# Performance work log

Measured on AMD Instinct MI355X. Metric: run time of the kernel, lower is better.

The kernel has to match this reference:

```python
import jax, jax.numpy as jnp
import numpy as np

# ---- static config (mirrors GaussianLSS __init__) ----
ORF_H, ORF_W = 256, 704
FC, FH, FW = 128, 32, 88
D_ST, D_END, D_STEP = 4.0, 45.0, 1.0
OUT_C = 128
ERROR_TOL = 1.0
OPACITY_THR = 0.05
XB = (-50.0, 50.0, 1.0)
YB = (-50.0, 50.0, 1.0)
BEV_H = int(round((YB[1] - YB[0]) / YB[2]))
BEV_W = int(round((XB[1] - XB[0]) / XB[2]))
DS = np.arange(D_ST, D_END, D_STEP, dtype=np.float32)
D = DS.shape[0]  # 41
BN_EPS = 1e-3
CHUNK = 512      # gaussians composited per scan step (16896 = 33*512)
B, NCAM = 1, 6


def make_frustum():
    ds = jnp.broadcast_to(jnp.asarray(DS)[:, None, None], (D, FH, FW))
    xs = jnp.broadcast_to(jnp.linspace(0.0, ORF_W - 1.0, FW)[None, None, :], (D, FH, FW))
    ys = jnp.broadcast_to(jnp.linspace(0.0, ORF_H - 1.0, FH)[None, :, None], (D, FH, FW))
    return jnp.stack([xs, ys, ds], -1)  # [D,FH,FW,3]


def get_geometry(rots, trans, intrins, post_rots, post_trans):
    fr = make_frustum()
    pts = fr[None, None] - post_trans[:, :, None, None, None, :]
    pts = jnp.einsum('bnij,bndhwj->bndhwi', jnp.linalg.inv(post_rots), pts)
    pts = jnp.concatenate([pts[..., :2] * pts[..., 2:3], pts[..., 2:3]], -1)
    comb = jnp.einsum('bnij,bnjk->bnik', rots, jnp.linalg.inv(intrins))
    pts = jnp.einsum('bnij,bndhwj->bndhwi', comb, pts) + trans[:, :, None, None, None, :]
    return pts  # [B,N,D,FH,FW,3] ego-frame frustum points


def conv2d(x, w, b, pad):
    y = jax.lax.conv_general_dilated(x, w, (1, 1), [(pad, pad), (pad, pad)],
                                     dimension_numbers=('NCHW', 'OIHW', 'NCHW'))
    return y + b[None, :, None, None]


def bnorm(x, g, bt, m, v):
    s = (g / jnp.sqrt(v + BN_EPS))[None, :, None, None]
    return (x - m[None, :, None, None]) * s + bt[None, :, None, None]


def splat(means, cov6, colors, ops, valid_in):
    # Differentiable BEV gaussian rasterization (3DGS math, orthographic BEV camera,
    # all depths equal -> compositing in stable gaussian-index order).
    H, W = BEV_H, BEV_W
    sh, sw = H / 2.0, W / 2.0  # h/h_meters with FoV=2 (BEVCamera)
    my = -sh * means[:, 1] + H / 2.0  # pixel row (full_proj_transform row 0)
    mx = -sw * means[:, 0] + W / 2.0  # pixel col (row 1)
    a = sh * sh * cov6[:, 3] + 0.3    # 2D cov = J Sigma_xy J^T, +0.3 low-pass as in 3DGS
    c = sw * sw * cov6[:, 0] + 0.3
    b = sh * sw * cov6[:, 1]
    det = a * c - b * b
    valid = valid_in & (det > 0)
    inv_det = jnp.where(det > 0, 1.0 / det, 0.0)
    cA, cB, cC = c * inv_det, -b * inv_det, a * inv_det
    pi = jnp.repeat(jnp.arange(H, dtype=jnp.float32), W)  # [P] pixel rows
    pj = jnp.tile(jnp.arange(W, dtype=jnp.float32), H)    # [P] pixel cols
    G = means.shape[0]
    nchunk = G // CHUNK
    resh = lambda x: x.reshape((nchunk, CHUNK) + x.shape[1:])
    chunks = (resh(my), resh(mx), resh(cA), resh(cB), resh(cC),
              resh(ops), resh(valid), resh(colors))

    def body(carry, ch):
        logT, acc = carry
        my_c, mx_c, A, Bc, Cc, op_c, val_c, col_c = ch
        dI = pi[None, :] - my_c[:, None]                     # [Gc,P]
        dJ = pj[None, :] - mx_c[:, None]
        q = A[:, None] * dI * dI + 2.0 * Bc[:, None] * dI * dJ + Cc[:, None] * dJ * dJ
        alpha = jnp.minimum(0.99, op_c[:, None] * jnp.exp(-0.5 * q))
        alpha = jnp.where(val_c[:, None] & (q >= 0) & (alpha >= 1.0 / 255.0), alpha, 0.0)
        log1m = jnp.log1p(-alpha)
        cum = jnp.cumsum(log1m, axis=0)
        T = jnp.exp(logT[None, :] + cum - log1m)             # transmittance before each gaussian
        acc = acc + jnp.einsum('gp,gc->pc', alpha * T, col_c)
        return (logT + cum[-1], acc), None

    P = H * W
    init = (jnp.zeros((P,), jnp.float32), jnp.zeros((P, colors.shape[1]), jnp.float32))
    (_, acc), _ = jax.lax.scan(jax.checkpoint(body), init, chunks)
    return acc.reshape(H, W, -1).transpose(2, 0, 1)  # [C,H,W], bg is zeros


def _forward(cam2ego_rot, cam2ego_trans, cam_intrins, post_cam2ego_rot, post_cam2ego_trans,
             img_feats, conv1_w, conv1_b, bn1_g, bn1_b, bn1_m, bn1_v,
             conv2_w, conv2_b, bn2_g, bn2_b, bn2_m, bn2_v, conv3_w, conv3_b):
    geom = get_geometry(cam2ego_rot, cam2ego_trans, cam_intrins, post_cam2ego_rot, post_cam2ego_trans)
    b, n = img_feats.shape[:2]
    x = img_feats.reshape(b * n, FC, FH, FW)
    x = jax.nn.relu(bnorm(conv2d(x, conv1_w, conv1_b, 1), bn1_g, bn1_b, bn1_m, bn1_v))
    x = jax.nn.relu(bnorm(conv2d(x, conv2_w, conv2_b, 1), bn2_g, bn2_b, bn2_m, bn2_v))
    x = conv2d(x, conv3_w, conv3_b, 0)
    depth_prob = jax.nn.softmax(x[:, :D], axis=1).reshape(b, n, D, FH, FW)
    opac = jax.nn.sigmoid(x[:, D:D + 1]).reshape(b, n, FH, FW)
    feats = x[:, D + 1:].reshape(b, n, OUT_C, FH, FW)
    # per-pixel gaussian moments of the depth distribution (compute_gaussian)
    means = jnp.einsum('bndhw,bndhwi->bnhwi', depth_prob, geom)
    delta = means[:, :, None] - geom                                       # [B,N,D,FH,FW,3]
    cov = jnp.einsum('bndhw,bndhwi,bndhwj->bnhwij', depth_prob, delta, delta) * (ERROR_TOL ** 2 / 9.0)
    center = jnp.array([(XB[0] + XB[1]) / 2.0, (YB[0] + YB[1]) / 2.0, 0.0], jnp.float32)
    scale = jnp.array([2.0 / (XB[1] - XB[0]), 2.0 / (YB[1] - YB[0]), 1.0], jnp.float32)
    m_n = (means - center) * scale
    cov_n = cov * (scale[:, None] * scale[None, :])
    cov6 = jnp.stack([cov_n[..., 0, 0], cov_n[..., 0, 1], cov_n[..., 0, 2],
                      cov_n[..., 1, 1], cov_n[..., 1, 2], cov_n[..., 2, 2]], -1)
    g = n * FH * FW
    colors = feats.transpose(0, 1, 3, 4, 2).reshape(b, g, OUT_C)
    m_n = m_n.reshape(b, g, 3)
    cov6 = cov6.reshape(b, g, 6)
    ops = opac.reshape(b, g)
    mask = ops > OPACITY_THR  # opacity filtering == zero contribution, order preserved
    bev = jax.vmap(splat)(m_n, cov6, colors, ops, mask)                    # [B,C,H,W]
    num_gaussians = mask.astype(jnp.float32).sum(-1).mean()
    return bev, num_gaussians


def setup_inputs():
    key = jax.random.key(0)
    ks = jax.random.split(key, 8)
    # camera-to-ego rotations: cam->ego axis permutation composed with per-camera yaw
    yaw = np.linspace(0.0, 2.0 * np.pi, NCAM, endpoint=False).astype(np.float32)
    cz, sz = np.cos(yaw), np.sin(yaw)
    rotz = np.zeros((NCAM, 3, 3), np.float32)
    rotz[:, 0, 0] = cz; rotz[:, 0, 1] = -sz
    rotz[:, 1, 0] = sz; rotz[:, 1, 1] = cz
    rotz[:, 2, 2] = 1.0
    perm = np.array([[0.0, 0.0, 1.0], [-1.0, 0.0, 0.0], [0.0, -1.0, 0.0]], np.float32)
    rots = np.einsum('nij,jk->nik', rotz, perm)
    cam2ego_rot = jnp.asarray(np.broadcast_to(rots, (B, NCAM, 3, 3)).copy())
    cam2ego_trans = jax.random.normal(ks[0], (B, NCAM, 3), jnp.float32)
    K = np.array([[600.0, 0.0, ORF_W / 2.0], [0.0, 600.0, ORF_H / 2.0], [0.0, 0.0, 1.0]], np.float32)
    cam_intrins = jnp.asarray(np.broadcast_to(K, (B, NCAM, 3, 3)).copy())
    post_cam2ego_rot = jnp.broadcast_to(jnp.eye(3, dtype=jnp.float32), (B, NCAM, 3, 3)) + jnp.zeros((B, NCAM, 3, 3), jnp.float32)
    post_cam2ego_trans = jnp.zeros((B, NCAM, 3), jnp.float32)
    img_feats = jax.random.normal(ks[1], (B, NCAM, FC, FH, FW), jnp.float32)
    def conv_init(k, o, i, kh, kw):
        return jax.random.normal(k, (o, i, kh, kw), jnp.float32) * (1.0 / np.sqrt(i * kh * kw))
    return dict(cam2ego_rot=cam2ego_rot, cam2ego_trans=cam2ego_trans, cam_intrins=cam_intrins,
                post_cam2ego_rot=post_cam2ego_rot, post_cam2ego_trans=post_cam2ego_trans,
                img_feats=img_feats,
                conv1_w=conv_init(ks[2], FC, FC, 3, 3), conv1_b=jnp.zeros((FC,), jnp.float32),
                bn1_g=jnp.ones((FC,), jnp.float32), bn1_b=jnp.zeros((FC,), jnp.float32),
                bn1_m=jnp.zeros((FC,), jnp.float32), bn1_v=jnp.ones((FC,), jnp.float32),
                conv2_w=conv_init(ks[3], FC, FC, 3, 3), conv2_b=jnp.zeros((FC,), jnp.float32),
                bn2_g=jnp.ones((FC,), jnp.float32), bn2_b=jnp.zeros((FC,), jnp.float32),
                bn2_m=jnp.zeros((FC,), jnp.float32), bn2_v=jnp.ones((FC,), jnp.float32),
                conv3_w=conv_init(ks[4], OUT_C + D + 1, FC, 1, 1),
                conv3_b=jax.random.normal(ks[5], (OUT_C + D + 1,), jnp.float32) * 0.1)


def reference(cam2ego_rot, cam2ego_trans, cam_intrins, post_cam2ego_rot, post_cam2ego_trans,
              img_feats, conv1_w, conv1_b, bn1_g, bn1_b, bn1_m, bn1_v,
              conv2_w, conv2_b, bn2_g, bn2_b, bn2_m, bn2_v, conv3_w, conv3_b):
    return _forward(cam2ego_rot, cam2ego_trans, cam_intrins, post_cam2ego_rot, post_cam2ego_trans,
                    img_feats, conv1_w, conv1_b, bn1_g, bn1_b, bn1_m, bn1_v,
                    conv2_w, conv2_b, bn2_g, bn2_b, bn2_m, bn2_v, conv3_w, conv3_b)
```

## Files before the change

kernel.cpp:

```cpp
#include <hip/hip_runtime.h>

#define NCAM 6
#define FC   128
#define FH_  32
#define FW_  88
#define NPIX (FH_*FW_)
#define PH   34
#define PW   92
#define PPIX (PH*PW)
#define ND   41
#define X3D  42
#define OUTC 128
#define GTOT (NCAM*NPIX)
#define BEVH 100
#define BEVW 100
#define NPXB (BEVH*BEVW)
#define NTILE 25
#define NWORD 264
#define NMASKW (NTILE*NTILE*NWORD)
#define WCAP  70000
#define CSIZE 64
#define CBLK  2048

#define SZA     (NCAM*FC*PPIX)
#define WS_CAM  0
#define WS_A    256
#define WS_RB   (WS_A  + SZA)
#define WS_X3   (WS_RB + SZA)
#define WS_GS   (WS_X3 + NCAM*X3D*NPIX)
#define WS_WL   (WS_GS + GTOT*8)
#define WS_BASE (WS_WL + WCAP)

__device__ inline void inv3x3(const float* m, float* o) {
    float a=m[0],b=m[1],c=m[2],d=m[3],e=m[4],f=m[5],g=m[6],h=m[7],i=m[8];
    float A=e*i-f*h, B=c*h-b*i, C=b*f-c*e;
    float Dd=f*g-d*i, E=a*i-c*g, F=c*d-a*f;
    float Gg=d*h-e*g, H=b*g-a*h, I=a*e-b*d;
    float r = 1.0f/(a*A + b*Dd + c*Gg);
    o[0]=A*r; o[1]=B*r; o[2]=C*r; o[3]=Dd*r; o[4]=E*r; o[5]=F*r;
    o[6]=Gg*r; o[7]=H*r; o[8]=I*r;
}

__global__ __launch_bounds__(256) void pad_input_kernel(const float* __restrict__ src,
        float* __restrict__ dst, float* __restrict__ rb,
        float* __restrict__ outp, unsigned long long* __restrict__ masks) {
    int idx = blockIdx.x*256 + threadIdx.x;
    if (idx < NMASKW) masks[idx] = 0ull;
    if (idx <= NPXB*OUTC) outp[idx] = 0.0f;
    if (idx >= NCAM*FC*PPIX) return;
    int plane = idx / PPIX, pp = idx - plane*PPIX;
    int y = pp / PW, x = pp - y*PW;
    bool interior = (y >= 1 && y <= FH_ && x >= 1 && x <= FW_);
    float v = 0.0f;
    if (interior)
        v = src[(size_t)plane*NPIX + (y-1)*FW_ + (x-1)];
    dst[idx] = v;
    if (!interior) rb[idx] = 0.0f;
}

__global__ __launch_bounds__(128) void conv3x3_pf_kernel(
        const float* __restrict__ in, float* __restrict__ out, const float* __restrict__ w,
        const float* __restrict__ cb, const float* __restrict__ bg, const float* __restrict__ bb,
        const float* __restrict__ bm, const float* __restrict__ bv) {
    const int n   = blockIdx.x;
    const int co0 = blockIdx.y * 4;
    const int qid = blockIdx.z * 128 + threadIdx.x;
    if (qid >= 704) return;
    const int y = qid / 22, x0 = (qid - y*22) * 4;
    float scale[4], shift[4];
    #pragma unroll
    for (int c=0;c<4;c++) {
        float s = bg[co0+c] * rsqrtf(bv[co0+c] + 1e-3f);
        scale[c] = s;
        shift[c] = (cb[co0+c] - bm[co0+c]) * s + bb[co0+c];
    }
    float acc[4][4] = {};
    const float* ip = in + (size_t)n*FC*PPIX + y*PW + x0;
    const float* wb = w + (size_t)co0*FC*9;
    float4 p4[3]; float2 p2[3];
    #pragma unroll
    for (int r=0;r<3;r++) {
        p4[r] = *(const float4*)(ip + r*PW);
        p2[r] = *(const float2*)(ip + r*PW + 4);
    }
    for (int ci=0; ci<FC; ++ci) {
        float v[3][6];
        #pragma unroll
        for (int r=0;r<3;r++) {
            v[r][0]=p4[r].x; v[r][1]=p4[r].y; v[r][2]=p4[r].z; v[r][3]=p4[r].w;
            v[r][4]=p2[r].x; v[r][5]=p2[r].y;
        }
        if (ci + 1 < FC) {
            const float* ipn = ip + PPIX;
            #pragma unroll
            for (int r=0;r<3;r++) {
                p4[r] = *(const float4*)(ipn + r*PW);
                p2[r] = *(const float2*)(ipn + r*PW + 4);
            }
        }
        #pragma unroll
        for (int c=0;c<4;c++) {
            const float* wr = wb + (size_t)c*FC*9 + ci*9;
            float w00=wr[0],w01=wr[1],w02=wr[2],w10=wr[3],w11=wr[4],
                  w12=wr[5],w20=wr[6],w21=wr[7],w22=wr[8];
            #pragma unroll
            for (int p=0;p<4;p++) {
                float a = acc[c][p];
                a = fmaf(w00, v[0][p], a); a = fmaf(w01, v[0][p+1], a); a = fmaf(w02, v[0][p+2], a);
                a = fmaf(w10, v[1][p], a); a = fmaf(w11, v[1][p+1], a); a = fmaf(w12, v[1][p+2], a);
                a = fmaf(w20, v[2][p], a); a = fmaf(w21, v[2][p+1], a); a = fmaf(w22, v[2][p+2], a);
                acc[c][p] = a;
            }
        }
        ip += PPIX;
    }
    const int po = (y+1)*PW + (x0+1);
    #pragma unroll
    for (int c=0;c<4;c++) {
        float* op = out + ((size_t)n*FC + co0 + c)*PPIX + po;
        #pragma unroll
        for (int p=0;p<4;p++)
            op[p] = fmaxf(fmaf(acc[c][p], scale[c], shift[c]), 0.0f);
    }
}

__global__ __launch_bounds__(256) void conv1x1_kernel(const float* __restrict__ in,
        float* __restrict__ x3d, float* __restrict__ colors,
        const float* __restrict__ w, const float* __restrict__ b) {
    const int n   = blockIdx.x;
    const int px  = blockIdx.y * 256 + threadIdx.x;
    const int y   = px / FW_, x = px - y*FW_;
    const int pp  = (y+1)*PW + (x+1);
    const float* ip = in + (size_t)n*FC*PPIX + pp;
    if (blockIdx.z < 6) {
        const int co0 = blockIdx.z * 7;
        const float* wr[7];
        float acc[7];
        #pragma unroll
        for (int k=0;k<7;k++) {
            int co = co0 + k;
            wr[k]  = w + (size_t)co*FC;
            acc[k] = b[co];
        }
        #pragma unroll 4
        for (int ci=0; ci<FC; ++ci) {
            float v = ip[(size_t)ci*PPIX];
            #pragma unroll
            for (int k=0;k<7;k++) acc[k] = fmaf(wr[k][ci], v, acc[k]);
        }
        #pragma unroll
        for (int k=0;k<7;k++)
            x3d[((size_t)n*X3D + co0 + k)*NPIX + px] = acc[k];
    } else {
        const int c0  = (blockIdx.z - 6) * 8;
        const int co0 = X3D + c0;
        const float* wr[8];
        float acc[8];
        #pragma unroll
        for (int k=0;k<8;k++) {
            int co = co0 + k;
            wr[k]  = w + (size_t)co*FC;
            acc[k] = b[co];
        }
        #pragma unroll 4
        for (int ci=0; ci<FC; ++ci) {
            float v = ip[(size_t)ci*PPIX];
            #pragma unroll
            for (int k=0;k<8;k++) acc[k] = fmaf(wr[k][ci], v, acc[k]);
        }
        float* cp = colors + (((size_t)(n*NPIX + px)) << 7) + c0;
        *(float4*)(cp)     = make_float4(acc[0], acc[1], acc[2], acc[3]);
        *(float4*)(cp + 4) = make_float4(acc[4], acc[5], acc[6], acc[7]);
    }
}

__global__ __launch_bounds__(256) void moments_kernel(const float* __restrict__ x3,
        const float* __restrict__ rot, const float* __restrict__ tr,
        const float* __restrict__ intr, const float* __restrict__ prot,
        const float* __restrict__ ptr_, float* __restrict__ gauss,
        float* __restrict__ ng) {
    __shared__ float cc[24];
    const int n = blockIdx.x / 11;
    if (threadIdx.x == 0) {
        float M1[9], Ki[9];
        inv3x3(prot + n*9, M1);
        inv3x3(intr + n*9, Ki);
        const float* R = rot + n*9;
        #pragma unroll
        for (int i=0;i<9;i++) cc[i] = M1[i];
        #pragma unroll
        for (int i=0;i<3;i++) cc[9+i] = ptr_[n*3+i];
        #pragma unroll
        for (int i=0;i<3;i++)
            #pragma unroll
            for (int j=0;j<3;j++)
                cc[12+i*3+j] = R[i*3+0]*Ki[0+j] + R[i*3+1]*Ki[3+j] + R[i*3+2]*Ki[6+j];
        #pragma unroll
        for (int i=0;i<3;i++) cc[21+i] = tr[n*3+i];
    }
    __syncthreads();
    const int gi = blockIdx.x*256 + threadIdx.x;
    const int p  = gi - n*NPIX;
    const int h  = p / FW_, xp = p - h*FW_;
    float u = xp * (703.0f/87.0f);
    float v = h  * (255.0f/31.0f);
    float fx = u - cc[9], fy = v - cc[10], fz = -cc[11];
    float p0x = cc[0]*fx + cc[1]*fy + cc[2]*fz;
    float p0y = cc[3]*fx + cc[4]*fy + cc[5]*fz;
    float p0z = cc[6]*fx + cc[7]*fy + cc[8]*fz;
    const float* lg = x3 + (size_t)n*X3D*NPIX + p;

    float lgv[ND];
    #pragma unroll
    for (int d=0; d<ND; ++d) lgv[d] = lg[(size_t)d*NPIX];

    float mxl = -1e30f;
    #pragma unroll
    for (int d=0; d<ND; ++d) mxl = fmaxf(mxl, lgv[d]);

    float s=0.f, sgx=0.f, sgy=0.f;
    #pragma unroll
    for (int d=0; d<ND; ++d) {
        float e  = __expf(lgv[d] - mxl);
        lgv[d] = e;
        float dz = 4.0f + (float)d;
        float pz = p0z + dz*cc[8];
        float px = (p0x + dz*cc[2]) * pz;
        float py = (p0y + dz*cc[5]) * pz;
        float gx = cc[12]*px + cc[13]*py + cc[14]*pz + cc[21];
        float gy = cc[15]*px + cc[16]*py + cc[17]*pz + cc[22];
        s += e; sgx += e*gx; sgy += e*gy;
    }
    float inv_s = 1.0f/s;
    float mex = sgx*inv_s, mey = sgy*inv_s;
    float cxx=0.f, cxy=0.f, cyy=0.f;
    #pragma unroll
    for (int d=0; d<ND; ++d) {
        float e  = lgv[d];
        float dz = 4.0f + (float)d;
        float pz = p0z + dz*cc[8];
        float px = (p0x + dz*cc[2]) * pz;
        float py = (p0y + dz*cc[5]) * pz;
        float gx = cc[12]*px + cc[13]*py + cc[14]*pz + cc[21];
        float gy = cc[15]*px + cc[16]*py + cc[17]*pz + cc[22];
        float dxv = gx - mex, dyv = gy - mey;
        cxx += e*dxv*dxv; cxy += e*dxv*dyv; cyy += e*dyv*dyv;
    }
    const float k9 = inv_s * (1.0f/9.0f);
    cxx *= k9; cxy *= k9; cyy *= k9;

    float lo = lg[(size_t)ND*NPIX];
    float op = 1.0f/(1.0f + __expf(-lo));
    bool mask = op > 0.05f;

    const float SC = 0.02f, SH = 50.0f, SW = 50.0f;
    float my = -SH*(mey*SC) + 50.0f;
    float mx = -SW*(mex*SC) + 50.0f;
    float a  = SH*SH*(cyy*SC*SC) + 0.3f;
    float b  = SH*SW*(cxy*SC*SC);
    float c  = SW*SW*(cxx*SC*SC) + 0.3f;
    float det = a*c - b*b;
    bool valid = mask && (det > 0.0f);
    float A, B2, C, qm, ri, rj;
    if (valid) {
        float idet = 1.0f/det;
        A = c*idet; B2 = -2.0f*b*idet; C = a*idet;
        qm = 2.0f*__logf(255.0f*op);
        ri = sqrtf(qm*a); rj = sqrtf(qm*c);
    } else { A=B2=C=0.f; qm=-1.0f; ri=-1e30f; rj=-1e30f; }
    float* gp = gauss + (size_t)gi*8;
    gp[0]=my; gp[1]=mx; gp[2]=A; gp[3]=B2; gp[4]=C; gp[5]=qm; gp[6]=ri; gp[7]=rj;

    unsigned long long bal = __ballot(mask);
    if ((threadIdx.x & 63) == 0) atomicAdd(ng, (float)__popcll(bal));
}

__global__ __launch_bounds__(256) void scatter_masks_kernel(const float* __restrict__ gauss,
        unsigned long long* __restrict__ masks) {
    const int idx = blockIdx.x*256 + threadIdx.x;
    const int g = idx >> 2, q = idx & 3;
    const float4 g0 = *(const float4*)(gauss + ((size_t)g << 3));
    const float4 g1 = *(const float4*)(gauss + ((size_t)g << 3) + 4);
    if (g1.y < 0.0f) return;
    const float my = g0.x, mx = g0.y, A = g0.z, B = 0.5f*g0.w, C = g1.x, qm = g1.y, ri = g1.z;
    const float invC = 1.0f / C;
    const float k2 = C*A - B*B;
    int ti0 = max(0, (int)floorf((my - ri) * 0.25f));
    int ti1 = min(NTILE-1, (int)floorf((my + ri) * 0.25f));
    int len = ti1 - ti0 + 1;
    int ta = ti0 + (len*q) / 4;
    int tb = ti0 + (len*(q+1)) / 4;
    const int wi = g >> 6;
    const unsigned long long bit = 1ull << (g & 63);
    for (int ti = ta; ti < tb; ++ti) {
        float jmn = 1e30f, jmx = -1e30f;
        #pragma unroll
        for (int r = 0; r < 4; ++r) {
            int i = 4*ti + r;
            if (i < 0 || i > 99) continue;
            float di = (float)i - my;
            float disc = C*qm - k2*di*di;
            if (disc < 0.0f) continue;
            float sd = sqrtf(disc);
            float jc = -B*di;
            jmn = fminf(jmn, (jc - sd)*invC + mx);
            jmx = fmaxf(jmx, (jc + sd)*invC + mx);
        }
        if (jmx < jmn) continue;
        int jl = max(0, (int)ceilf(jmn));
        int jh = min(99, (int)floorf(jmx));
        if (jl > jh) continue;
        for (int tj = (jl >> 2); tj <= (jh >> 2); ++tj)
            atomicOr(&masks[(size_t)(ti*NTILE + tj)*NWORD + wi], bit);
    }
}

__global__ __launch_bounds__(256) void cnt_kernel(const unsigned long long* __restrict__ masks,
                                                  int* __restrict__ cnt) {
    __shared__ int sc;
    const int tile = blockIdx.x, t = threadIdx.x;
    if (t == 0) sc = 0;
    __syncthreads();
    if (t < NWORD) atomicAdd(&sc, __popcll(masks[(size_t)tile*NWORD + t]));
    __syncthreads();
    if (t == 0) cnt[tile] = sc;
}

__global__ __launch_bounds__(640) void scan_kernel(const int* __restrict__ cnt,
        int* __restrict__ off, int* __restrict__ choff, int* __restrict__ nwork) {
    __shared__ int wsum[16], wsum2[16];
    const int t = threadIdx.x;
    const int lane = t & 63, wv = t >> 6;
    int c  = (t < NTILE*NTILE) ? cnt[t] : 0;
    int ch = (c + CSIZE-1) >> 6;
    int v = c, v2 = ch;
    #pragma unroll
    for (int o = 1; o < 64; o <<= 1) {
        int u  = __shfl_up(v,  (unsigned)o, 64);
        int u2 = __shfl_up(v2, (unsigned)o, 64);
        if (lane >= o) { v += u; v2 += u2; }
    }
    if (lane == 63) { wsum[wv] = v; wsum2[wv] = v2; }
    __syncthreads();
    int pre = 0, pre2 = 0;
    for (int w2 = 0; w2 < wv; ++w2) { pre += wsum[w2]; pre2 += wsum2[w2]; }
    int inc = v + pre, inc2 = v2 + pre2;
    if (t < NTILE*NTILE) { off[t] = inc - c; choff[t] = inc2 - ch; }
    if (t == NTILE*NTILE - 1) {
        off[NTILE*NTILE] = inc;
        choff[NTILE*NTILE] = inc2;
        nwork[0] = (inc2 > WCAP) ? WCAP : inc2;
    }
}

__global__ __launch_bounds__(256) void fill_kernel(const unsigned long long* __restrict__ masks,
        const int* __restrict__ cnt, const int* __restrict__ off, const int* __restrict__ choff,
        unsigned short* __restrict__ list, int* __restrict__ wl) {
    __shared__ unsigned long long sw[NWORD];
    __shared__ int wpre[NWORD];
    const int tile = blockIdx.x, t = threadIdx.x;
    if (t < NWORD) sw[t] = masks[(size_t)tile*NWORD + t];
    __syncthreads();
    if (t == 0) {
        int run = 0;
        for (int w2 = 0; w2 < NWORD; ++w2) { wpre[w2] = run; run += __popcll(sw[w2]); }
    }
    __syncthreads();
    if (t < NWORD) {
        unsigned long long m = sw[t];
        int pos = off[tile] + wpre[t], base = t << 6;
        while (m) { int b = __builtin_ctzll(m); m &= m - 1; list[pos++] = (unsigned short)(base + b); }
    }
    int nch = (cnt[tile] + CSIZE-1)/CSIZE;
    int c0 = choff[tile];
    if (t < nch && c0 + t < WCAP) wl[c0 + t] = (tile << 9) | t;
}

__device__ inline float eval_alpha(const float4 g0, const float4 g1, float fi, float fj) {
    float dI = fi - g0.x, dJ = fj - g0.y;
    float q = dI*(g0.z*dI + g0.w*dJ) + g1.x*dJ*dJ;
    if (q < 0.0f || q > g1.y) return 0.0f;
    return fminf(0.99f, 0.003921568627f * __expf(0.5f*(g1.y - q)));
}

__global__ __launch_bounds__(256) void chunk_sums_kernel(const float* __restrict__ gauss,
        const unsigned short* __restrict__ list, const int* __restrict__ cnt,
        const int* __restrict__ off, const int* __restrict__ wl, const int* __restrict__ nwork,
        float* __restrict__ base) {
    const int nw = nwork[0];
    const int lane = threadIdx.x & 63;
    const int wid  = (blockIdx.x * 256 + threadIdx.x) >> 6;
    const int nwv  = (gridDim.x * 256) >> 6;
    const int px = lane & 15, kg = lane >> 4;
    for (int e = wid; e < nw; e += nwv) {
        int v = wl[e], tile = v >> 9, c = v & 511;
        int hbase = off[tile] + (c << 6);
        int nh = min(CSIZE, cnt[tile] - (c << 6));
        const int i0 = (tile / NTILE) * 4, j0 = (tile % NTILE) * 4;
        const float fi = (float)(i0 + (px >> 2)), fj = (float)(j0 + (px & 3));
        float s = 1.0f;
        for (int k = kg; k < nh; k += 4) {
            int g = list[hbase + k];
            float4 g0 = *(const float4*)(gauss + ((size_t)g << 3));
            float4 g1 = *(const float4*)(gauss + ((size_t)g << 3) + 4);
            float a = eval_alpha(g0, g1, fi, fj);
            s *= (1.0f - a);
        }
        s *= __shfl_xor(s, 16, 64);
        s *= __shfl_xor(s, 32, 64);
        if (lane < 16) base[(size_t)e*16 + lane] = s;
    }
}

__global__ __launch_bounds__(256) void chunk_prefix_kernel(const int* __restrict__ choff,
                                                           float* __restrict__ base) {
    __shared__ float part[16][17];
    const int tile = blockIdx.x, t = threadIdx.x;
    const int c0 = choff[tile], nch = choff[tile+1] - c0;
    if (nch == 0) return;
    const int px = t & 15, cg = t >> 4;
    const int L16 = (nch + 15) >> 4;
    const int a0 = cg*L16, a1 = min(nch, a0 + L16);
    float s = 1.0f;
    for (int c = a0; c < a1; ++c) s *= base[(size_t)(c0 + c)*16 + px];
    part[cg][px] = s;
    __syncthreads();
    if (t < 16) {
        float run = 1.0f;
        #pragma unroll
        for (int k = 0; k < 16; ++k) { float tmp = part[k][t]; part[k][t] = run; run *= tmp; }
    }
    __syncthreads();
    float run = part[cg][px];
    for (int c = a0; c < a1; ++c) {
        size_t idx = (size_t)(c0 + c)*16 + px;
        float tmp = base[idx];
        base[idx] = run;
        run *= tmp;
    }
}

__global__ __launch_bounds__(256) void composite_kernel(const float* __restrict__ gauss,
        const float* __restrict__ colors, const unsigned short* __restrict__ list,
        const int* __restrict__ cnt, const int* __restrict__ off, const int* __restrict__ wl,
        const int* __restrict__ nwork, const float* __restrict__ base, float* __restrict__ out) {
    const int nw = nwork[0];
    const int t = threadIdx.x;
    const int lane = t & 63;
    const int e_px = t >> 4, e_kg = t & 15;
    const int cs4 = t & 31;
    const int par = (t >> 5) & 1;
    const int pq  = t >> 6;
    const int f_pxq = t >> 5;
    const int f_r0  = f_pxq >> 2, f_j = f_pxq & 3;
    __shared__ unsigned short slist[2][CSIZE];
    __shared__ float s_w[CSIZE][17];
    __shared__ float fred[128*17];
    const int per = (nw + CBLK - 1) / CBLK;
    int e0 = blockIdx.x * per;
    if (e0 >= nw) return;
    int e1 = min(nw, e0 + per);

    float4 acc[4];
    #pragma unroll
    for (int j=0;j<4;j++) acc[j] = make_float4(0.f,0.f,0.f,0.f);
    int cur_tile = wl[e0] >> 9;
    int cur_i0 = (cur_tile / NTILE) * 4, cur_j0 = (cur_tile % NTILE) * 4;

    int buf = 0;
    {
        int v = wl[e0], tl = v >> 9, c = v & 511;
        int nh0 = min(CSIZE, cnt[tl] - (c << 6));
        if (t < nh0) slist[0][t] = list[off[tl] + (c << 6) + t];
    }

    for (int e = e0; e < e1; ++e) {
        int v = wl[e], tile = v >> 9, c = v & 511;
        const bool tflush = (tile != cur_tile);
        const int fi0 = cur_i0, fj0 = cur_j0;
        if (tflush) {
            #pragma unroll
            for (int j = 0; j < 4; ++j) {
                acc[j].x += __shfl_xor(acc[j].x, 32, 64);
                acc[j].y += __shfl_xor(acc[j].y, 32, 64);
                acc[j].z += __shfl_xor(acc[j].z, 32, 64);
                acc[j].w += __shfl_xor(acc[j].w, 32, 64);
            }
            if (par == 0) {
                float* fr = &fred[(pq*32 + cs4)*17];
                #pragma unroll
                for (int j = 0; j < 4; ++j) {
                    fr[(j<<2)+0] = acc[j].x; fr[(j<<2)+1] = acc[j].y;
                    fr[(j<<2)+2] = acc[j].z; fr[(j<<2)+3] = acc[j].w;
                }
            }
            #pragma unroll
            for (int j=0;j<4;j++) acc[j] = make_float4(0.f,0.f,0.f,0.f);
            cur_tile = tile;
            cur_i0 = (tile / NTILE) * 4; cur_j0 = (tile % NTILE) * 4;
        }
        const int nh = min(CSIZE, cnt[tile] - (c << 6));
        __syncthreads();
        if (tflush) {
            const float* f0 = &fred[(f_r0*32 + cs4)*17 + (f_j<<2)];
            const float* f1 = &fred[((f_r0+2)*32 + cs4)*17 + (f_j<<2)];
            const int pix0 = (fi0 + f_r0) * BEVW + fj0 + f_j;
            const int pix1 = pix0 + 2 * BEVW;
            float* op = out + (size_t)(cs4 << 2) * NPXB;
            atomicAdd(op + 0*NPXB + pix0, f0[0]); atomicAdd(op + 1*NPXB + pix0, f0[1]);
            atomicAdd(op + 2*NPXB + pix0, f0[2]); atomicAdd(op + 3*NPXB + pix0, f0[3]);
            atomicAdd(op + 0*NPXB + pix1, f1[0]); atomicAdd(op + 1*NPXB + pix1, f1[1]);
            atomicAdd(op + 2*NPXB + pix1, f1[2]); atomicAdd(op + 3*NPXB + pix1, f1[3]);
        }
        if (e + 1 < e1) {
            int v2 = wl[e+1], tl2 = v2 >> 9, c2 = v2 & 511;
            int nh2 = min(CSIZE, cnt[tl2] - (c2 << 6));
            if (t < nh2) slist[buf^1][t] = list[off[tl2] + (c2 << 6) + t];
        }
        {
            const float fi = (float)(cur_i0 + (e_px >> 2)), fj = (float)(cur_j0 + (e_px & 3));
            const int k0 = e_kg << 2;
            float a4[4]; float p = 1.0f;
            #pragma unroll
            for (int i = 0; i < 4; ++i) {
                int k = k0 + i;
                float a = 0.0f;
                if (k < nh) {
                    int g = slist[buf][k];
                    float4 g0 = *(const float4*)(gauss + ((size_t)g << 3));
                    float4 g1 = *(const float4*)(gauss + ((size_t)g << 3) + 4);
                    a = eval_alpha(g0, g1, fi, fj);
                }
                a4[i] = a;
                p *= (1.0f - a);
            }
            float s = p;
            #pragma unroll
            for (int o = 1; o < 16; o <<= 1) {
                float u = __shfl_up(s, (unsigned)o, 64);
                if ((lane & 15) >= o) s *= u;
            }
            float ex = __shfl_up(s, 1u, 64);
            float T = base[(size_t)e*16 + e_px] * (((lane & 15) == 0) ? 1.0f : ex);
            #pragma unroll
            for (int i = 0; i < 4; ++i) {
                float wv = a4[i] * T; T -= wv;
                s_w[k0 + i][e_px] = wv;
            }
        }
        __syncthreads();
        if (nh == CSIZE) {
            #pragma unroll 8
            for (int k = 0; k < CSIZE/2; ++k) {
                const int idx = (k << 1) | par;
                int g = slist[buf][idx];
                const float* swr = s_w[idx] + (pq << 2);
                float w0 = swr[0], w1 = swr[1], w2 = swr[2], w3 = swr[3];
                float4 cl = *(const float4*)(colors + ((size_t)g << 7) + (cs4 << 2));
                acc[0].x = fmaf(w0, cl.x, acc[0].x); acc[0].y = fmaf(w0, cl.y, acc[0].y);
                acc[0].z = fmaf(w0, cl.z, acc[0].z); acc[0].w = fmaf(w0, cl.w, acc[0].w);
                acc[1].x = fmaf(w1, cl.x, acc[1].x); acc[1].y = fmaf(w1, cl.y, acc[1].y);
                acc[1].z = fmaf(w1, cl.z, acc[1].z); acc[1].w = fmaf(w1, cl.w, acc[1].w);
                acc[2].x = fmaf(w2, cl.x, acc[2].x); acc[2].y = fmaf(w2, cl.y, acc[2].y);
                acc[2].z = fmaf(w2, cl.z, acc[2].z); acc[2].w = fmaf(w2, cl.w, acc[2].w);
                acc[3].x = fmaf(w3, cl.x, acc[3].x); acc[3].y = fmaf(w3, cl.y, acc[3].y);
                acc[3].z = fmaf(w3, cl.z, acc[3].z); acc[3].w = fmaf(w3, cl.w, acc[3].w);
            }
        } else {
            #pragma unroll 4
            for (int k = 0; k < CSIZE/2; ++k) {
                const int idx = (k << 1) | par;
                if (idx >= nh) break;
                int g = slist[buf][idx];
                const float* swr = s_w[idx] + (pq << 2);
                float w0 = swr[0], w1 = swr[1], w2 = swr[2], w3 = swr[3];
                float4 cl = *(const float4*)(colors + ((size_t)g << 7) + (cs4 << 2));
                acc[0].x = fmaf(w0, cl.x, acc[0].x); acc[0].y = fmaf(w0, cl.y, acc[0].y);
                acc[0].z = fmaf(w0, cl.z, acc[0].z); acc[0].w = fmaf(w0, cl.w, acc[0].w);
                acc[1].x = fmaf(w1, cl.x, acc[1].x); acc[1].y = fmaf(w1, cl.y, acc[1].y);
                acc[1].z = fmaf(w1, cl.z, acc[1].z); acc[1].w = fmaf(w1, cl.w, acc[1].w);
                acc[2].x = fmaf(w2, cl.x, acc[2].x); acc[2].y = fmaf(w2, cl.y, acc[2].y);
                acc[2].z = fmaf(w2, cl.z, acc[2].z); acc[2].w = fmaf(w2, cl.w, acc[2].w);
                acc[3].x = fmaf(w3, cl.x, acc[3].x); acc[3].y = fmaf(w3, cl.y, acc[3].y);
                acc[3].z = fmaf(w3, cl.z, acc[3].z); acc[3].w = fmaf(w3, cl.w, acc[3].w);
            }
        }
        buf ^= 1;
    }
    #pragma unroll
    for (int j = 0; j < 4; ++j) {
        acc[j].x += __shfl_xor(acc[j].x, 32, 64);
        acc[j].y += __shfl_xor(acc[j].y, 32, 64);
        acc[j].z += __shfl_xor(acc[j].z, 32, 64);
        acc[j].w += __shfl_xor(acc[j].w, 32, 64);
    }
    if (par == 0) {
        float* fr = &fred[(pq*32 + cs4)*17];
        #pragma unroll
        for (int j = 0; j < 4; ++j) {
            fr[(j<<2)+0] = acc[j].x; fr[(j<<2)+1] = acc[j].y;
            fr[(j<<2)+2] = acc[j].z; fr[(j<<2)+3] = acc[j].w;
        }
    }
    __syncthreads();
    {
        const float* f0 = &fred[(f_r0*32 + cs4)*17 + (f_j<<2)];
        const float* f1 = &fred[((f_r0+2)*32 + cs4)*17 + (f_j<<2)];
        const int pix0 = (cur_i0 + f_r0) * BEVW + cur_j0 + f_j;
        const int pix1 = pix0 + 2 * BEVW;
        float* op = out + (size_t)(cs4 << 2) * NPXB;
        atomicAdd(op + 0*NPXB + pix0, f0[0]); atomicAdd(op + 1*NPXB + pix0, f0[1]);
        atomicAdd(op + 2*NPXB + pix0, f0[2]); atomicAdd(op + 3*NPXB + pix0, f0[3]);
        atomicAdd(op + 0*NPXB + pix1, f1[0]); atomicAdd(op + 1*NPXB + pix1, f1[1]);
        atomicAdd(op + 2*NPXB + pix1, f1[2]); atomicAdd(op + 3*NPXB + pix1, f1[3]);
    }
}

extern "C" void kernel_launch(void* const* d_in, const int* in_sizes, int n_in,
                              void* d_out, int out_size, void* d_ws, size_t ws_size,
                              hipStream_t stream) {
    const float* rot  = (const float*)d_in[0];
    const float* tr   = (const float*)d_in[1];
    const float* intr = (const float*)d_in[2];
    const float* prot = (const float*)d_in[3];
    const float* ptr_ = (const float*)d_in[4];
    const float* img  = (const float*)d_in[5];
    const float* c1w  = (const float*)d_in[6];  const float* c1b = (const float*)d_in[7];
    const float* b1g  = (const float*)d_in[8];  const float* b1b = (const float*)d_in[9];
    const float* b1m  = (const float*)d_in[10]; const float* b1v = (const float*)d_in[11];
    const float* c2w  = (const float*)d_in[12]; const float* c2b = (const float*)d_in[13];
    const float* b2g  = (const float*)d_in[14]; const float* b2b = (const float*)d_in[15];
    const float* b2m  = (const float*)d_in[16]; const float* b2v = (const float*)d_in[17];
    const float* c3w  = (const float*)d_in[18]; const float* c3b = (const float*)d_in[19];
    float* out = (float*)d_out;
    float* ws  = (float*)d_ws;
    float* RA  = ws + WS_A;
    float* RB  = ws + WS_RB;
    float* X3B = ws + WS_X3;
    float* GS  = ws + WS_GS;
    int*   WL  = (int*)(ws + WS_WL);
    float* BASE = ws + WS_BASE;
    unsigned long long* MASKS = (unsigned long long*)BASE;
    int* AUXI = (int*)(ws + WS_X3 + 330000);
    int* CNT = AUXI;
    int* OFF = AUXI + 640;
    int* CHOFF = AUXI + 1280;
    int* NWORK = AUXI + 1920;
    unsigned short* LIST = (unsigned short*)RA;
    float* COL = RB;
    float* ngp = out + (size_t)NPXB*OUTC;

    pad_input_kernel<<<(NCAM*FC*PPIX + 255)/256, 256, 0, stream>>>(img, RA, RB, out, MASKS);
    conv3x3_pf_kernel<<<dim3(NCAM,32,6), 128, 0, stream>>>(RA, RB, c1w, c1b, b1g, b1b, b1m, b1v);
    conv3x3_pf_kernel<<<dim3(NCAM,32,6), 128, 0, stream>>>(RB, RA, c2w, c2b, b2g, b2b, b2m, b2v);
    conv1x1_kernel<<<dim3(NCAM,11,22), 256, 0, stream>>>(RA, X3B, COL, c3w, c3b);
    moments_kernel<<<GTOT/256, 256, 0, stream>>>(X3B, rot, tr, intr, prot, ptr_, GS, ngp);
    scatter_masks_kernel<<<GTOT*4/256, 256, 0, stream>>>(GS, MASKS);
    cnt_kernel<<<NTILE*NTILE, 256, 0, stream>>>(MASKS, CNT);
    scan_kernel<<<1, 640, 0, stream>>>(CNT, OFF, CHOFF, NWORK);
    fill_kernel<<<NTILE*NTILE, 256, 0, stream>>>(MASKS, CNT, OFF, CHOFF, LIST, WL);
    chunk_sums_kernel<<<8192, 256, 0, stream>>>(GS, LIST, CNT, OFF, WL, NWORK, BASE);
    chunk_prefix_kernel<<<NTILE*NTILE, 256, 0, stream>>>(CHOFF, BASE);
    composite_kernel<<<CBLK, 256, 0, stream>>>(GS, COL, LIST, CNT, OFF, WL, NWORK, BASE, out);
}
```

Measured before the change: 463.6 us.

## Composite gaussians with bf16 MFMA and store colors as bf16

```diff
diff --git a/kernel.cpp b/kernel.cpp
--- a/kernel.cpp
+++ b/kernel.cpp
@@ -31,6 +31,15 @@
 #define WS_WL   (WS_GS + GTOT*8)
 #define WS_BASE (WS_WL + WCAP)
 
+typedef __attribute__((ext_vector_type(8))) short bf16x8;
+typedef __attribute__((ext_vector_type(4))) float f32x4;
+
+__device__ inline unsigned short f2bf(float f) {
+    unsigned u = __float_as_uint(f);
+    u += 0x7fffu + ((u >> 16) & 1u);
+    return (unsigned short)(u >> 16);
+}
+
 __device__ inline void inv3x3(const float* m, float* o) {
     float a=m[0],b=m[1],c=m[2],d=m[3],e=m[4],f=m[5],g=m[6],h=m[7],i=m[8];
     float A=e*i-f*h, B=c*h-b*i, C=b*f-c*e;
@@ -125,7 +134,7 @@
 }
 
 __global__ __launch_bounds__(256) void conv1x1_kernel(const float* __restrict__ in,
-        float* __restrict__ x3d, float* __restrict__ colors,
+        float* __restrict__ x3d, unsigned short* __restrict__ colors16,
         const float* __restrict__ w, const float* __restrict__ b) {
     const int n   = blockIdx.x;
     const int px  = blockIdx.y * 256 + threadIdx.x;
@@ -168,9 +177,15 @@
             #pragma unroll
             for (int k=0;k<8;k++) acc[k] = fmaf(wr[k][ci], v, acc[k]);
         }
-        float* cp = colors + (((size_t)(n*NPIX + px)) << 7) + c0;
-        *(float4*)(cp)     = make_float4(acc[0], acc[1], acc[2], acc[3]);
-        *(float4*)(cp + 4) = make_float4(acc[4], acc[5], acc[6], acc[7]);
+        unsigned short h[8];
+        #pragma unroll
+        for (int k=0;k<8;k++) h[k] = f2bf(acc[k]);
+        uint4 pk;
+        pk.x = (unsigned)h[0] | ((unsigned)h[1] << 16);
+        pk.y = (unsigned)h[2] | ((unsigned)h[3] << 16);
+        pk.z = (unsigned)h[4] | ((unsigned)h[5] << 16);
+        pk.w = (unsigned)h[6] | ((unsigned)h[7] << 16);
+        *(uint4*)(colors16 + (((size_t)(n*NPIX + px)) << 7) + c0) = pk;
     }
 }
 
@@ -441,29 +456,31 @@
 }
 
 __global__ __launch_bounds__(256) void composite_kernel(const float* __restrict__ gauss,
-        const float* __restrict__ colors, const unsigned short* __restrict__ list,
+        const unsigned short* __restrict__ colors16, const unsigned short* __restrict__ list,
         const int* __restrict__ cnt, const int* __restrict__ off, const int* __restrict__ wl,
         const int* __restrict__ nwork, const float* __restrict__ base, float* __restrict__ out) {
     const int nw = nwork[0];
     const int t = threadIdx.x;
     const int lane = t & 63;
     const int e_px = t >> 4, e_kg = t & 15;
-    const int cs4 = t & 31;
-    const int par = (t >> 5) & 1;
-    const int pq  = t >> 6;
+    const int wv_id = t >> 6;
+    const int m16 = lane & 15;
+    const int kb  = lane >> 4;
+    const int chA = (wv_id << 5) + m16;
+    const int chB = chA + 16;
     const int f_pxq = t >> 5;
     const int f_r0  = f_pxq >> 2, f_j = f_pxq & 3;
+    const int cs4r  = t & 31;
     __shared__ unsigned short slist[2][CSIZE];
-    __shared__ float s_w[CSIZE][17];
+    __shared__ unsigned short s_w16[8][16][8];
     __shared__ float fred[128*17];
     const int per = (nw + CBLK - 1) / CBLK;
     int e0 = blockIdx.x * per;
     if (e0 >= nw) return;
     int e1 = min(nw, e0 + per);
 
-    float4 acc[4];
-    #pragma unroll
-    for (int j=0;j<4;j++) acc[j] = make_float4(0.f,0.f,0.f,0.f);
+    f32x4 accA = {0.f,0.f,0.f,0.f};
+    f32x4 accB = {0.f,0.f,0.f,0.f};
     int cur_tile = wl[e0] >> 9;
     int cur_i0 = (cur_tile / NTILE) * 4, cur_j0 = (cur_tile % NTILE) * 4;
 
@@ -471,7 +488,7 @@
     {
         int v = wl[e0], tl = v >> 9, c = v & 511;
         int nh0 = min(CSIZE, cnt[tl] - (c << 6));
-        if (t < nh0) slist[0][t] = list[off[tl] + (c << 6) + t];
+        if (t < CSIZE) slist[0][t] = (t < nh0) ? list[off[tl] + (c << 6) + t] : 0;
     }
 
     for (int e = e0; e < e1; ++e) {
@@ -479,34 +496,26 @@
         const bool tflush = (tile != cur_tile);
         const int fi0 = cur_i0, fj0 = cur_j0;
         if (tflush) {
-            #pragma unroll
-            for (int j = 0; j < 4; ++j) {
-                acc[j].x += __shfl_xor(acc[j].x, 32, 64);
-                acc[j].y += __shfl_xor(acc[j].y, 32, 64);
-                acc[j].z += __shfl_xor(acc[j].z, 32, 64);
-                acc[j].w += __shfl_xor(acc[j].w, 32, 64);
+            const int cs4A = (wv_id << 3) + (m16 >> 2);
+            const int compA = m16 & 3;
+            #pragma unroll
+            for (int r = 0; r < 4; ++r) {
+                fred[((kb << 5) + cs4A)*17 + (r << 2) + compA]     = accA[r];
+                fred[((kb << 5) + cs4A + 4)*17 + (r << 2) + compA] = accB[r];
             }
-            if (par == 0) {
-                float* fr = &fred[(pq*32 + cs4)*17];
-                #pragma unroll
-                for (int j = 0; j < 4; ++j) {
-                    fr[(j<<2)+0] = acc[j].x; fr[(j<<2)+1] = acc[j].y;
-                    fr[(j<<2)+2] = acc[j].z; fr[(j<<2)+3] = acc[j].w;
-                }
-            }
-            #pragma unroll
-            for (int j=0;j<4;j++) acc[j] = make_float4(0.f,0.f,0.f,0.f);
+            accA = (f32x4){0.f,0.f,0.f,0.f};
+            accB = (f32x4){0.f,0.f,0.f,0.f};
             cur_tile = tile;
             cur_i0 = (tile / NTILE) * 4; cur_j0 = (tile % NTILE) * 4;
         }
         const int nh = min(CSIZE, cnt[tile] - (c << 6));
         __syncthreads();
         if (tflush) {
-            const float* f0 = &fred[(f_r0*32 + cs4)*17 + (f_j<<2)];
-            const float* f1 = &fred[((f_r0+2)*32 + cs4)*17 + (f_j<<2)];
+            const float* f0 = &fred[(f_r0*32 + cs4r)*17 + (f_j<<2)];
+            const float* f1 = &fred[((f_r0+2)*32 + cs4r)*17 + (f_j<<2)];
             const int pix0 = (fi0 + f_r0) * BEVW + fj0 + f_j;
             const int pix1 = pix0 + 2 * BEVW;
-            float* op = out + (size_t)(cs4 << 2) * NPXB;
+            float* op = out + (size_t)(cs4r << 2) * NPXB;
             atomicAdd(op + 0*NPXB + pix0, f0[0]); atomicAdd(op + 1*NPXB + pix0, f0[1]);
             atomicAdd(op + 2*NPXB + pix0, f0[2]); atomicAdd(op + 3*NPXB + pix0, f0[3]);
             atomicAdd(op + 0*NPXB + pix1, f1[0]); atomicAdd(op + 1*NPXB + pix1, f1[1]);
@@ -515,7 +524,7 @@
         if (e + 1 < e1) {
             int v2 = wl[e+1], tl2 = v2 >> 9, c2 = v2 & 511;
             int nh2 = min(CSIZE, cnt[tl2] - (c2 << 6));
-            if (t < nh2) slist[buf^1][t] = list[off[tl2] + (c2 << 6) + t];
+            if (t < CSIZE) slist[buf^1][t] = (t < nh2) ? list[off[tl2] + (c2 << 6) + t] : 0;
         }
         {
             const float fi = (float)(cur_i0 + (e_px >> 2)), fj = (float)(cur_j0 + (e_px & 3));
@@ -542,73 +551,49 @@
             }
             float ex = __shfl_up(s, 1u, 64);
             float T = base[(size_t)e*16 + e_px] * (((lane & 15) == 0) ? 1.0f : ex);
+            unsigned short* swp = &s_w16[e_kg >> 1][e_px][(e_kg & 1) << 2];
             #pragma unroll
             for (int i = 0; i < 4; ++i) {
-                float wv = a4[i] * T; T -= wv;
-                s_w[k0 + i][e_px] = wv;
+                float wvv = a4[i] * T; T -= wvv;
+                swp[i] = f2bf(wvv);
             }
         }
         __syncthreads();
-        if (nh == CSIZE) {
-            #pragma unroll 8
-            for (int k = 0; k < CSIZE/2; ++k) {
-                const int idx = (k << 1) | par;
-                int g = slist[buf][idx];
-                const float* swr = s_w[idx] + (pq << 2);
-                float w0 = swr[0], w1 = swr[1], w2 = swr[2], w3 = swr[3];
-                float4 cl = *(const float4*)(colors + ((size_t)g << 7) + (cs4 << 2));
-                acc[0].x = fmaf(w0, cl.x, acc[0].x); acc[0].y = fmaf(w0, cl.y, acc[0].y);
-                acc[0].z = fmaf(w0, cl.z, acc[0].z); acc[0].w = fmaf(w0, cl.w, acc[0].w);
-                acc[1].x = fmaf(w1, cl.x, acc[1].x); acc[1].y = fmaf(w1, cl.y, acc[1].y);
-                acc[1].z = fmaf(w1, cl.z, acc[1].z); acc[1].w = fmaf(w1, cl.w, acc[1].w);
-                acc[2].x = fmaf(w2, cl.x, acc[2].x); acc[2].y = fmaf(w2, cl.y, acc[2].y);
-                acc[2].z = fmaf(w2, cl.z, acc[2].z); acc[2].w = fmaf(w2, cl.w, acc[2].w);
-                acc[3].x = fmaf(w3, cl.x, acc[3].x); acc[3].y = fmaf(w3, cl.y, acc[3].y);
-                acc[3].z = fmaf(w3, cl.z, acc[3].z); acc[3].w = fmaf(w3, cl.w, acc[3].w);
+        {
+            #pragma unroll
+            for (int s = 0; s < 2; ++s) {
+                bf16x8 afrag = *(const bf16x8*)&s_w16[(s << 2) + kb][m16][0];
+                const int kbase = (s << 5) + (kb << 3);
+                bf16x8 bA, bB;
+                #pragma unroll
+                for (int j = 0; j < 8; ++j) {
+                    int g = slist[buf][kbase + j];
+                    const unsigned short* cp = colors16 + ((size_t)g << 7);
+                    bA[j] = (short)cp[chA];
+                    bB[j] = (short)cp[chB];
+                }
+                accA = __builtin_amdgcn_mfma_f32_16x16x32_bf16(afrag, bA, accA, 0, 0, 0);
+                accB = __builtin_amdgcn_mfma_f32_16x16x32_bf16(afrag, bB, accB, 0, 0, 0);
             }
-        } else {
-            #pragma unroll 4
-            for (int k = 0; k < CSIZE/2; ++k) {
-                const int idx = (k << 1) | par;
-                if (idx >= nh) break;
-                int g = slist[buf][idx];
-                const float* swr = s_w[idx] + (pq << 2);
-                float w0 = swr[0], w1 = swr[1], w2 = swr[2], w3 = swr[3];
-                float4 cl = *(const float4*)(colors + ((size_t)g << 7) + (cs4 << 2));
-                acc[0].x = fmaf(w0, cl.x, acc[0].x); acc[0].y = fmaf(w0, cl.y, acc[0].y);
-                acc[0].z = fmaf(w0, cl.z, acc[0].z); acc[0].w = fmaf(w0, cl.w, acc[0].w);
-                acc[1].x = fmaf(w1, cl.x, acc[1].x); acc[1].y = fmaf(w1, cl.y, acc[1].y);
-                acc[1].z = fmaf(w1, cl.z, acc[1].z); acc[1].w = fmaf(w1, cl.w, acc[1].w);
-                acc[2].x = fmaf(w2, cl.x, acc[2].x); acc[2].y = fmaf(w2, cl.y, acc[2].y);
-                acc[2].z = fmaf(w2, cl.z, acc[2].z); acc[2].w = fmaf(w2, cl.w, acc[2].w);
-                acc[3].x = fmaf(w3, cl.x, acc[3].x); acc[3].y = fmaf(w3, cl.y, acc[3].y);
-                acc[3].z = fmaf(w3, cl.z, acc[3].z); acc[3].w = fmaf(w3, cl.w, acc[3].w);
-            }
         }
         buf ^= 1;
     }
-    #pragma unroll
-    for (int j = 0; j < 4; ++j) {
-        acc[j].x += __shfl_xor(acc[j].x, 32, 64);
-        acc[j].y += __shfl_xor(acc[j].y, 32, 64);
-        acc[j].z += __shfl_xor(acc[j].z, 32, 64);
-        acc[j].w += __shfl_xor(acc[j].w, 32, 64);
-    }
-    if (par == 0) {
-        float* fr = &fred[(pq*32 + cs4)*17];
-        #pragma unroll
-        for (int j = 0; j < 4; ++j) {
-            fr[(j<<2)+0] = acc[j].x; fr[(j<<2)+1] = acc[j].y;
-            fr[(j<<2)+2] = acc[j].z; fr[(j<<2)+3] = acc[j].w;
-        }
-    }
-    __syncthreads();
     {
-        const float* f0 = &fred[(f_r0*32 + cs4)*17 + (f_j<<2)];
-        const float* f1 = &fred[((f_r0+2)*32 + cs4)*17 + (f_j<<2)];
+        const int cs4A = (wv_id << 3) + (m16 >> 2);
+        const int compA = m16 & 3;
+        #pragma unroll
+        for (int r = 0; r < 4; ++r) {
+            fred[((kb << 5) + cs4A)*17 + (r << 2) + compA]     = accA[r];
+            fred[((kb << 5) + cs4A + 4)*17 + (r << 2) + compA] = accB[r];
+        }
+    }
+    __syncthreads();
+    {
+        const float* f0 = &fred[(f_r0*32 + cs4r)*17 + (f_j<<2)];
+        const float* f1 = &fred[((f_r0+2)*32 + cs4r)*17 + (f_j<<2)];
         const int pix0 = (cur_i0 + f_r0) * BEVW + cur_j0 + f_j;
         const int pix1 = pix0 + 2 * BEVW;
-        float* op = out + (size_t)(cs4 << 2) * NPXB;
+        float* op = out + (size_t)(cs4r << 2) * NPXB;
         atomicAdd(op + 0*NPXB + pix0, f0[0]); atomicAdd(op + 1*NPXB + pix0, f0[1]);
         atomicAdd(op + 2*NPXB + pix0, f0[2]); atomicAdd(op + 3*NPXB + pix0, f0[3]);
         atomicAdd(op + 0*NPXB + pix1, f1[0]); atomicAdd(op + 1*NPXB + pix1, f1[1]);
@@ -647,13 +632,13 @@
     int* CHOFF = AUXI + 1280;
     int* NWORK = AUXI + 1920;
     unsigned short* LIST = (unsigned short*)RA;
-    float* COL = RB;
+    unsigned short* COL16 = (unsigned short*)RB;
     float* ngp = out + (size_t)NPXB*OUTC;
 
     pad_input_kernel<<<(NCAM*FC*PPIX + 255)/256, 256, 0, stream>>>(img, RA, RB, out, MASKS);
     conv3x3_pf_kernel<<<dim3(NCAM,32,6), 128, 0, stream>>>(RA, RB, c1w, c1b, b1g, b1b, b1m, b1v);
     conv3x3_pf_kernel<<<dim3(NCAM,32,6), 128, 0, stream>>>(RB, RA, c2w, c2b, b2g, b2b, b2m, b2v);
-    conv1x1_kernel<<<dim3(NCAM,11,22), 256, 0, stream>>>(RA, X3B, COL, c3w, c3b);
+    conv1x1_kernel<<<dim3(NCAM,11,22), 256, 0, stream>>>(RA, X3B, COL16, c3w, c3b);
     moments_kernel<<<GTOT/256, 256, 0, stream>>>(X3B, rot, tr, intr, prot, ptr_, GS, ngp);
     scatter_masks_kernel<<<GTOT*4/256, 256, 0, stream>>>(GS, MASKS);
     cnt_kernel<<<NTILE*NTILE, 256, 0, stream>>>(MASKS, CNT);
@@ -661,5 +646,5 @@
     fill_kernel<<<NTILE*NTILE, 256, 0, stream>>>(MASKS, CNT, OFF, CHOFF, LIST, WL);
     chunk_sums_kernel<<<8192, 256, 0, stream>>>(GS, LIST, CNT, OFF, WL, NWORK, BASE);
     chunk_prefix_kernel<<<NTILE*NTILE, 256, 0, stream>>>(CHOFF, BASE);
-    composite_kernel<<<CBLK, 256, 0, stream>>>(GS, COL, LIST, CNT, OFF, WL, NWORK, BASE, out);
-}
+    composite_kernel<<<CBLK, 256, 0, stream>>>(GS, COL16, LIST, CNT, OFF, WL, NWORK, BASE, out);
+}
```

New measurement: 456.6 us. Within noise of the previous version (-1.5%).
